# Kernel tuning notes

Measured on AMD Instinct MI355X. Metric: run time of the kernel, lower is better.

Reference implementation:

```python
import jax, jax.numpy as jnp
import numpy as np

N, E, A, D, B = 30000, 60000, 6, 16, 4096
F_IN, F_HID, F_EMB = 256, 256, 256
ALPHA = 0.2  # LeakyReLU negative slope


def _layer(node_embs, edge_embs, edge_list, node_list, Wn, We, ae, an, concat):
    out = Wn.shape[1]
    hn = node_embs @ Wn                      # [N, out]
    he = edge_embs @ We                      # [E, out]
    # stage 1: hyperedge update = attention over its member nodes
    gn = hn[edge_list]                       # [E, A, out] gather
    se = (he @ ae[:out])[:, None] + gn @ ae[out:]            # [E, A]
    att_e = jax.nn.softmax(jax.nn.leaky_relu(se, ALPHA), axis=1)
    new_edge = jnp.einsum('ea,eao->eo', att_e, gn)           # [E, out]
    # stage 2: node update = attention over its incident hyperedges
    ge = new_edge[node_list]                 # [N, D, out] gather
    sn = (hn @ an[:out])[:, None] + ge @ an[out:]            # [N, D]
    att_n = jax.nn.softmax(jax.nn.leaky_relu(sn, ALPHA), axis=1)
    new_node = jnp.einsum('nd,ndo->no', att_n, ge)           # [N, out]
    if concat:
        return jax.nn.elu(new_node), jax.nn.elu(new_edge)
    return new_node, new_edge


def setup_inputs() -> dict:
    key = jax.random.key(0)
    ks = jax.random.split(key, 16)
    s = 0.1
    return {
        'batch_inputs': jax.random.randint(ks[0], (B, A + 1), 0, N),
        'node_embs': jax.random.normal(ks[1], (N, F_IN), jnp.float32),
        'edge_embs': jax.random.normal(ks[2], (E, F_IN), jnp.float32),
        'edge_list': jax.random.randint(ks[3], (E, A), 0, N),
        'node_list': jax.random.randint(ks[4], (N, D), 0, E),
        'Wn1': jax.random.normal(ks[5], (F_IN, F_HID), jnp.float32) * s,
        'We1': jax.random.normal(ks[6], (F_IN, F_HID), jnp.float32) * s,
        'ae1': jax.random.normal(ks[7], (2 * F_HID,), jnp.float32) * s,
        'an1': jax.random.normal(ks[8], (2 * F_HID,), jnp.float32) * s,
        'Wn2': jax.random.normal(ks[9], (F_HID, F_EMB), jnp.float32) * s,
        'We2': jax.random.normal(ks[10], (F_HID, F_EMB), jnp.float32) * s,
        'ae2': jax.random.normal(ks[11], (2 * F_EMB,), jnp.float32) * s,
        'an2': jax.random.normal(ks[12], (2 * F_EMB,), jnp.float32) * s,
    }


def reference(batch_inputs, node_embs, edge_embs, edge_list, node_list,
              Wn1, We1, ae1, an1, Wn2, We2, ae2, an2):
    # single attention head (nheads=1), concat=True -> ELU; dropout identity (eval)
    n1, e1 = _layer(node_embs, edge_embs, edge_list, node_list, Wn1, We1, ae1, an1, True)
    n2, e2 = _layer(n1, e1, edge_list, node_list, Wn2, We2, ae2, an2, False)
    n2, e2 = jax.nn.elu(n2), jax.nn.elu(e2)
    # assemble: slot 0 = hyperedge embedding, slots 1..right-1 = node embeddings
    S = batch_inputs.shape[1]
    cols = jnp.arange(S - 1)
    nz = batch_inputs[:, :-1] != 0
    right = jnp.max(jnp.where(nz, cols, -1), axis=1) + 1      # [B]
    pos = jnp.arange(S)
    mask = (pos[None, :] >= 1) & (pos[None, :] < right[:, None])  # [B, S]
    gathered = n2[batch_inputs]                               # [B, S, F_EMB]
    out = jnp.where(mask[:, :, None], gathered, jnp.float32(0))
    out = out.at[:, 0, :].set(e2[batch_inputs[:, 0]])
    return out
```

## Files before the change

kernel.cpp:

```cpp
#include <hip/hip_runtime.h>
#include <stdint.h>

typedef unsigned short u16;
typedef unsigned int   u32;
typedef __attribute__((ext_vector_type(8))) short bf16x8;
typedef __attribute__((ext_vector_type(4))) float f32x4;

#define N_NODES 30000
#define N_EDGES 60000
#define A_DEG   6
#define D_DEG   16
#define BATCH   4096
#define FEAT    256
#define APAD    8

__device__ __forceinline__ float bfbits2f(u32 hi){ union{u32 u; float f;} v; v.u = hi; return v.f; }
__device__ __forceinline__ float bf2f(u16 h){ return bfbits2f(((u32)h)<<16); }
__device__ __forceinline__ u16 f2bf(float f){
  union{float f; u32 u;} v; v.f = f;
  u32 u = v.u;
  return (u16)((u + 0x7fffu + ((u>>16)&1u)) >> 16);
}

struct F4 { float x,y,z,w; };
struct F8 { float v[8]; };

__device__ __forceinline__ F4 load4(const float* p){
  float4 t = *reinterpret_cast<const float4*>(p);
  F4 f; f.x=t.x; f.y=t.y; f.z=t.z; f.w=t.w; return f;
}
__device__ __forceinline__ F4 load4(const u16* p){
  uint2 u = *reinterpret_cast<const uint2*>(p);
  F4 f;
  f.x = bfbits2f(u.x<<16);
  f.y = bfbits2f(u.x & 0xffff0000u);
  f.z = bfbits2f(u.y<<16);
  f.w = bfbits2f(u.y & 0xffff0000u);
  return f;
}
__device__ __forceinline__ F8 load8(const float* p){
  float4 a = *reinterpret_cast<const float4*>(p);
  float4 b = *reinterpret_cast<const float4*>(p+4);
  F8 f; f.v[0]=a.x; f.v[1]=a.y; f.v[2]=a.z; f.v[3]=a.w;
        f.v[4]=b.x; f.v[5]=b.y; f.v[6]=b.z; f.v[7]=b.w; return f;
}
__device__ __forceinline__ F8 load8(const u16* p){
  uint4 u = *reinterpret_cast<const uint4*>(p);
  F8 f;
  f.v[0]=bfbits2f(u.x<<16); f.v[1]=bfbits2f(u.x&0xffff0000u);
  f.v[2]=bfbits2f(u.y<<16); f.v[3]=bfbits2f(u.y&0xffff0000u);
  f.v[4]=bfbits2f(u.z<<16); f.v[5]=bfbits2f(u.z&0xffff0000u);
  f.v[6]=bfbits2f(u.w<<16); f.v[7]=bfbits2f(u.w&0xffff0000u);
  return f;
}
__device__ __forceinline__ void acc8(float* o, uint4 u, float ww){
  o[0] += ww*bfbits2f(u.x<<16); o[1] += ww*bfbits2f(u.x&0xffff0000u);
  o[2] += ww*bfbits2f(u.y<<16); o[3] += ww*bfbits2f(u.y&0xffff0000u);
  o[4] += ww*bfbits2f(u.z<<16); o[5] += ww*bfbits2f(u.z&0xffff0000u);
  o[6] += ww*bfbits2f(u.w<<16); o[7] += ww*bfbits2f(u.w&0xffff0000u);
}
__device__ __forceinline__ void store_bf8(u16* p, const float* f){
  uint4 u;
  u.x = (u32)f2bf(f[0]) | ((u32)f2bf(f[1])<<16);
  u.y = (u32)f2bf(f[2]) | ((u32)f2bf(f[3])<<16);
  u.z = (u32)f2bf(f[4]) | ((u32)f2bf(f[5])<<16);
  u.w = (u32)f2bf(f[6]) | ((u32)f2bf(f[7])<<16);
  *reinterpret_cast<uint4*>(p) = u;
}

__device__ __forceinline__ float eluf(float x){ return x > 0.f ? x : (__expf(x) - 1.f); }
__device__ __forceinline__ float lrelu(float x){ return x > 0.f ? x : 0.2f*x; }

__device__ __forceinline__ float wave_sum_lane0(float v){
  #pragma unroll
  for (int off = 32; off > 0; off >>= 1) v += __shfl_down(v, off, 64);
  return v;
}
__device__ __forceinline__ float half_sum_all(float v){
  #pragma unroll
  for (int off = 1; off < 32; off <<= 1) v += __shfl_xor(v, off, 64);
  return v;
}

__global__ __launch_bounds__(256) void prep_k(
    const float* __restrict__ Wn1, u16* __restrict__ Wt1,
    const float* __restrict__ Wn2, u16* __restrict__ Wt2,
    const float* __restrict__ We1, const float* __restrict__ ae1, float* __restrict__ wE1,
    const float* __restrict__ We2, const float* __restrict__ ae2, float* __restrict__ wE2)
{
  if (blockIdx.z < 2){
    const float* W = blockIdx.z ? Wn2 : Wn1;
    u16* Wt        = blockIdx.z ? Wt2 : Wt1;
    __shared__ float T[32][33];
    const int bx = blockIdx.x;
    const int by = blockIdx.y;
    const int tc = threadIdx.x & 31;
    const int tr = threadIdx.x >> 5;
    #pragma unroll
    for (int i=0;i<4;i++){
      int r = tr + i*8;
      T[r][tc] = W[(bx*32 + r)*FEAT + by*32 + tc];
    }
    __syncthreads();
    #pragma unroll
    for (int i=0;i<4;i++){
      int r = tr + i*8;
      Wt[(by*32 + r)*FEAT + bx*32 + tc] = f2bf(T[tc][r]);
    }
  } else {
    const int vb   = blockIdx.y*8 + blockIdx.x;
    const int lane = threadIdx.x & 63;
    const int row  = vb*4 + (threadIdx.x >> 6);
    const int c    = lane*4;
    {
      F4 h = load4(We1 + (long)row*FEAT + c);
      F4 a = load4(ae1 + c);
      float p = wave_sum_lane0(h.x*a.x + h.y*a.y + h.z*a.z + h.w*a.w);
      if (lane == 0) wE1[row] = p;
    }
    {
      F4 h = load4(We2 + (long)row*FEAT + c);
      F4 a = load4(ae2 + c);
      float p = wave_sum_lane0(h.x*a.x + h.y*a.y + h.z*a.z + h.w*a.w);
      if (lane == 0) wE2[row] = p;
    }
  }
}

template<bool ELU, typename TIN>
__global__ __launch_bounds__(256) void gemm_mfma_k(
    const TIN* __restrict__ X, const u16* __restrict__ Wt,
    const float* __restrict__ v1, const float* __restrict__ v2,
    u16* __restrict__ Y, float* __restrict__ hg, float* __restrict__ snb,
    int M)
{
  __shared__ u16 As[64][FEAT + APAD];
  __shared__ float hgs[64], sns[64];
  const int tid = threadIdx.x;
  const long row0 = (long)blockIdx.x * 64;

  if (tid < 64){ hgs[tid] = 0.f; sns[tid] = 0.f; }

  {
    const int c = (tid & 15) << 4;
    #pragma unroll
    for (int i=0;i<4;i++){
      const int r = (tid >> 4) + 16*i;
      u16* dst = &As[r][c];
      if (row0 + r < M){
        const TIN* src = X + (row0 + r)*FEAT + c;
        #pragma unroll
        for (int j=0;j<4;j++){
          F4 v = load4(src + 4*j);
          if (ELU){ v.x=eluf(v.x); v.y=eluf(v.y); v.z=eluf(v.z); v.w=eluf(v.w); }
          dst[4*j+0]=f2bf(v.x); dst[4*j+1]=f2bf(v.y);
          dst[4*j+2]=f2bf(v.z); dst[4*j+3]=f2bf(v.w);
        }
      } else {
        #pragma unroll
        for (int j=0;j<16;j++) dst[j] = 0;
      }
    }
  }
  __syncthreads();

  const int wave = tid >> 6;
  const int lane = tid & 63;
  const int l15  = lane & 15;
  const int kg   = lane >> 4;

  f32x4 acc[4][4] = {};

  for (int k0 = 0; k0 < FEAT; k0 += 32){
    bf16x8 a[4], b[4];
    #pragma unroll
    for (int rt=0;rt<4;rt++)
      a[rt] = *reinterpret_cast<const bf16x8*>(&As[rt*16 + l15][k0 + kg*8]);
    #pragma unroll
    for (int t=0;t<4;t++){
      const int n = wave*64 + t*16 + l15;
      b[t] = *reinterpret_cast<const bf16x8*>(Wt + (long)n*FEAT + k0 + kg*8);
    }
    #pragma unroll
    for (int rt=0;rt<4;rt++)
      #pragma unroll
      for (int t=0;t<4;t++)
        acc[rt][t] = __builtin_amdgcn_mfma_f32_16x16x32_bf16(a[rt], b[t], acc[rt][t], 0, 0, 0);
  }

  __syncthreads();

  float p1[4][4] = {}, p2[4][4] = {};
  #pragma unroll
  for (int t=0;t<4;t++){
    const int col = wave*64 + t*16 + l15;
    const float a1 = v1[col];
    const float a2 = v2[col];
    #pragma unroll
    for (int rt=0;rt<4;rt++){
      #pragma unroll
      for (int r=0;r<4;r++){
        const float val = acc[rt][t][r];
        As[rt*16 + kg*4 + r][col] = f2bf(val);
        p1[rt][r] += val * a1;
        p2[rt][r] += val * a2;
      }
    }
  }
  #pragma unroll
  for (int off=1; off<16; off<<=1){
    #pragma unroll
    for (int rt=0;rt<4;rt++)
      #pragma unroll
      for (int r=0;r<4;r++){
        p1[rt][r] += __shfl_xor(p1[rt][r], off, 64);
        p2[rt][r] += __shfl_xor(p2[rt][r], off, 64);
      }
  }
  if (l15 == 0){
    #pragma unroll
    for (int rt=0;rt<4;rt++)
      #pragma unroll
      for (int r=0;r<4;r++){
        atomicAdd(&hgs[rt*16 + kg*4 + r], p1[rt][r]);
        atomicAdd(&sns[rt*16 + kg*4 + r], p2[rt][r]);
      }
  }
  __syncthreads();

  {
    const int c = (tid & 15) << 4;
    #pragma unroll
    for (int i=0;i<4;i++){
      const int r = (tid >> 4) + 16*i;
      if (row0 + r < M){
        const uint4* s = reinterpret_cast<const uint4*>(&As[r][c]);
        uint4* d = reinterpret_cast<uint4*>(Y + (row0 + r)*FEAT + c);
        d[0] = s[0]; d[1] = s[1];
      }
    }
  }
  if (tid < 64 && row0 + tid < M){
    hg[row0 + tid]  = hgs[tid];
    snb[row0 + tid] = sns[tid];
  }
}

__global__ __launch_bounds__(256) void node_gemm_k(
    const u16* __restrict__ NE, const int* __restrict__ node_list,
    const float* __restrict__ snb1, const float* __restrict__ ned,
    const u16* __restrict__ Wt,
    const float* __restrict__ v1, const float* __restrict__ v2,
    u16* __restrict__ Y, float* __restrict__ hg, float* __restrict__ snb2,
    int M)
{
  __shared__ u16 As[64][FEAT + APAD];
  __shared__ float hgs[64], sns[64];
  const int tid = threadIdx.x;
  const long row0 = (long)blockIdx.x * 64;

  if (tid < 64){ hgs[tid] = 0.f; sns[tid] = 0.f; }

  const int hw = tid >> 5;
  const int hl = tid & 31;
  const int c  = hl*8;
  for (int i=0;i<4;i++){
    const int rA = hw*8 + 2*i;
    const int rB = rA + 1;
    const long nA = row0 + rA;
    const long nB = row0 + rB;
    u16* dstA = &As[rA][c];
    u16* dstB = &As[rB][c];
    if (nB < M){
      int idxA[D_DEG], idxB[D_DEG];
      #pragma unroll
      for (int d=0; d<D_DEG; d++) idxA[d] = node_list[nA*D_DEG + d];
      #pragma unroll
      for (int d=0; d<D_DEG; d++) idxB[d] = node_list[nB*D_DEG + d];
      float nvA[D_DEG], nvB[D_DEG];
      #pragma unroll
      for (int d=0; d<D_DEG; d++) nvA[d] = ned[idxA[d]];
      #pragma unroll
      for (int d=0; d<D_DEG; d++) nvB[d] = ned[idxB[d]];
      uint4 hbA[D_DEG], hbB[D_DEG];
      #pragma unroll
      for (int d=0; d<D_DEG; d++)
        hbA[d] = *reinterpret_cast<const uint4*>(NE + (long)idxA[d]*FEAT + c);
      #pragma unroll
      for (int d=0; d<D_DEG; d++)
        hbB[d] = *reinterpret_cast<const uint4*>(NE + (long)idxB[d]*FEAT + c);

      const float sbA = snb1[nA];
      const float sbB = snb1[nB];
      float wA[D_DEG], wB[D_DEG];
      float mxA = -1e30f, mxB = -1e30f;
      #pragma unroll
      for (int d=0; d<D_DEG; d++){
        float sA = lrelu(sbA + nvA[d]); wA[d] = sA; mxA = fmaxf(mxA, sA);
        float sB = lrelu(sbB + nvB[d]); wB[d] = sB; mxB = fmaxf(mxB, sB);
      }
      float sumA = 0.f, sumB = 0.f;
      #pragma unroll
      for (int d=0; d<D_DEG; d++){
        wA[d] = __expf(wA[d]-mxA); sumA += wA[d];
        wB[d] = __expf(wB[d]-mxB); sumB += wB[d];
      }
      const float invA = 1.f/sumA;
      const float invB = 1.f/sumB;

      float oA[8] = {};
      #pragma unroll
      for (int d=0; d<D_DEG; d++) acc8(oA, hbA[d], wA[d]*invA);
      #pragma unroll
      for (int j=0;j<8;j++) dstA[j] = f2bf(eluf(oA[j]));

      float oB[8] = {};
      #pragma unroll
      for (int d=0; d<D_DEG; d++) acc8(oB, hbB[d], wB[d]*invB);
      #pragma unroll
      for (int j=0;j<8;j++) dstB[j] = f2bf(eluf(oB[j]));
    } else {
      for (int t=0;t<2;t++){
        const long n = (t==0) ? nA : nB;
        u16* dst = (t==0) ? dstA : dstB;
        if (n < M){
          int idx[D_DEG];
          #pragma unroll
          for (int d=0; d<D_DEG; d++) idx[d] = node_list[n*D_DEG + d];
          float nv[D_DEG];
          #pragma unroll
          for (int d=0; d<D_DEG; d++) nv[d] = ned[idx[d]];
          uint4 hb[D_DEG];
          #pragma unroll
          for (int d=0; d<D_DEG; d++)
            hb[d] = *reinterpret_cast<const uint4*>(NE + (long)idx[d]*FEAT + c);
          const float sb = snb1[n];
          float w[D_DEG];
          float mx = -1e30f;
          #pragma unroll
          for (int d=0; d<D_DEG; d++){
            float s = lrelu(sb + nv[d]); w[d] = s; mx = fmaxf(mx, s);
          }
          float sum = 0.f;
          #pragma unroll
          for (int d=0; d<D_DEG; d++){ w[d] = __expf(w[d]-mx); sum += w[d]; }
          const float inv = 1.f/sum;
          float o[8] = {};
          #pragma unroll
          for (int d=0; d<D_DEG; d++) acc8(o, hb[d], w[d]*inv);
          #pragma unroll
          for (int j=0;j<8;j++) dst[j] = f2bf(eluf(o[j]));
        } else {
          #pragma unroll
          for (int j=0;j<8;j++) dst[j] = 0;
        }
      }
    }
  }
  __syncthreads();

  const int wave = tid >> 6;
  const int lane = tid & 63;
  const int l15  = lane & 15;
  const int kg   = lane >> 4;

  f32x4 acc[4][4] = {};

  for (int k0 = 0; k0 < FEAT; k0 += 32){
    bf16x8 a[4], b[4];
    #pragma unroll
    for (int rt=0;rt<4;rt++)
      a[rt] = *reinterpret_cast<const bf16x8*>(&As[rt*16 + l15][k0 + kg*8]);
    #pragma unroll
    for (int t=0;t<4;t++){
      const int n = wave*64 + t*16 + l15;
      b[t] = *reinterpret_cast<const bf16x8*>(Wt + (long)n*FEAT + k0 + kg*8);
    }
    #pragma unroll
    for (int rt=0;rt<4;rt++)
      #pragma unroll
      for (int t=0;t<4;t++)
        acc[rt][t] = __builtin_amdgcn_mfma_f32_16x16x32_bf16(a[rt], b[t], acc[rt][t], 0, 0, 0);
  }

  __syncthreads();

  float p1[4][4] = {}, p2[4][4] = {};
  #pragma unroll
  for (int t=0;t<4;t++){
    const int col = wave*64 + t*16 + l15;
    const float a1 = v1[col];
    const float a2 = v2[col];
    #pragma unroll
    for (int rt=0;rt<4;rt++){
      #pragma unroll
      for (int r=0;r<4;r++){
        const float val = acc[rt][t][r];
        As[rt*16 + kg*4 + r][col] = f2bf(val);
        p1[rt][r] += val * a1;
        p2[rt][r] += val * a2;
      }
    }
  }
  #pragma unroll
  for (int off=1; off<16; off<<=1){
    #pragma unroll
    for (int rt=0;rt<4;rt++)
      #pragma unroll
      for (int r=0;r<4;r++){
        p1[rt][r] += __shfl_xor(p1[rt][r], off, 64);
        p2[rt][r] += __shfl_xor(p2[rt][r], off, 64);
      }
  }
  if (l15 == 0){
    #pragma unroll
    for (int rt=0;rt<4;rt++)
      #pragma unroll
      for (int r=0;r<4;r++){
        atomicAdd(&hgs[rt*16 + kg*4 + r], p1[rt][r]);
        atomicAdd(&sns[rt*16 + kg*4 + r], p2[rt][r]);
      }
  }
  __syncthreads();

  {
    const int cc = (tid & 15) << 4;
    #pragma unroll
    for (int i=0;i<4;i++){
      const int r = (tid >> 4) + 16*i;
      if (row0 + r < M){
        const uint4* s = reinterpret_cast<const uint4*>(&As[r][cc]);
        uint4* d = reinterpret_cast<uint4*>(Y + (row0 + r)*FEAT + cc);
        d[0] = s[0]; d[1] = s[1];
      }
    }
  }
  if (tid < 64 && row0 + tid < M){
    hg[row0 + tid]   = hgs[tid];
    snb2[row0 + tid] = sns[tid];
  }
}

template<typename TIN, bool ELU, bool SB_PRE, bool SEB_OUT>
__global__ __launch_bounds__(256) void edge_attn_k(const u16* __restrict__ Hn,
    const TIN* __restrict__ Xe, const float* __restrict__ wE,
    const int* __restrict__ edge_list,
    const float* __restrict__ hg, const float* __restrict__ an_hi,
    const float* __restrict__ seb_in, const float* __restrict__ wE_nxt,
    float* __restrict__ seb_out,
    u16* __restrict__ NE, float* __restrict__ ned)
{
  const int tid = threadIdx.x;
  const int hl  = tid & 31;
  const int e   = blockIdx.x*8 + (tid >> 5);
  const int c   = hl*8;

  int idx[A_DEG];
  #pragma unroll
  for (int a=0;a<A_DEG;a++) idx[a] = edge_list[e*A_DEG + a];
  float hgv[A_DEG];
  #pragma unroll
  for (int a=0;a<A_DEG;a++) hgv[a] = hg[idx[a]];
  uint4 hb[A_DEG];
  #pragma unroll
  for (int a=0;a<A_DEG;a++)
    hb[a] = *reinterpret_cast<const uint4*>(Hn + (long)idx[a]*FEAT + c);

  float sb;
  if (SB_PRE){
    sb = seb_in[e];
  } else {
    F8 x = load8(Xe + (long)e*FEAT + c);
    if (ELU){
      #pragma unroll
      for (int j=0;j<8;j++) x.v[j] = eluf(x.v[j]);
    }
    F8 v = load8(wE + c);
    float p = 0.f;
    #pragma unroll
    for (int j=0;j<8;j++) p += x.v[j]*v.v[j];
    sb = half_sum_all(p);
  }

  float w[A_DEG];
  float mx = -1e30f;
  #pragma unroll
  for (int a=0;a<A_DEG;a++){
    float s = lrelu(sb + hgv[a]);
    w[a] = s; mx = fmaxf(mx, s);
  }
  float sum = 0.f;
  #pragma unroll
  for (int a=0;a<A_DEG;a++){ w[a] = __expf(w[a]-mx); sum += w[a]; }
  const float inv = 1.f/sum;

  float o[8] = {};
  #pragma unroll
  for (int a=0;a<A_DEG;a++) acc8(o, hb[a], w[a]*inv);
  store_bf8(NE + (long)e*FEAT + c, o);

  {
    F8 v = load8(an_hi + c);
    float p = 0.f;
    #pragma unroll
    for (int j=0;j<8;j++) p += o[j]*v.v[j];
    p = half_sum_all(p);
    if (hl == 0) ned[e] = p;
  }
  if (SEB_OUT){
    F8 v = load8(wE_nxt + c);
    float p = 0.f;
    #pragma unroll
    for (int j=0;j<8;j++) p += eluf(o[j])*v.v[j];
    p = half_sum_all(p);
    if (hl == 0) seb_out[e] = p;
  }
}

__global__ __launch_bounds__(256) void node_assemble_k(
    const u16* __restrict__ NE, const int* __restrict__ node_list,
    const float* __restrict__ snb, const float* __restrict__ ned,
    const int* __restrict__ batch, float* __restrict__ out)
{
  const int b   = blockIdx.x;
  const int tid = threadIdx.x;
  const int hw  = tid >> 5;
  const int hl  = tid & 31;
  const int c   = hl*8;

  int right = 0;
  #pragma unroll
  for (int cc=0; cc<6; cc++){ if (batch[b*7 + cc] != 0) right = cc+1; }

  if (hw == 6){
    const int e = batch[b*7 + 0];
    F8 x = load8(NE + (long)e*FEAT + c);
    float4 o0, o1;
    o0.x=eluf(x.v[0]); o0.y=eluf(x.v[1]); o0.z=eluf(x.v[2]); o0.w=eluf(x.v[3]);
    o1.x=eluf(x.v[4]); o1.y=eluf(x.v[5]); o1.z=eluf(x.v[6]); o1.w=eluf(x.v[7]);
    float* po = out + ((long)b*7 + 0)*FEAT + c;
    *reinterpret_cast<float4*>(po)   = o0;
    *reinterpret_cast<float4*>(po+4) = o1;
  } else if (hw < 6){
    const int s  = hw + 1;
    float* po = out + ((long)b*7 + s)*FEAT + c;
    if (s < right){
      const int n = batch[b*7 + s];
      int idx[D_DEG];
      #pragma unroll
      for (int d=0; d<D_DEG; d++) idx[d] = node_list[(long)n*D_DEG + d];
      float nv[D_DEG];
      #pragma unroll
      for (int d=0; d<D_DEG; d++) nv[d] = ned[idx[d]];
      const float sb = snb[n];
      float w[D_DEG];
      float mx = -1e30f;
      #pragma unroll
      for (int d=0; d<D_DEG; d++){
        float sc = lrelu(sb + nv[d]);
        w[d] = sc; mx = fmaxf(mx, sc);
      }
      float sum = 0.f;
      #pragma unroll
      for (int d=0; d<D_DEG; d++){ w[d] = __expf(w[d]-mx); sum += w[d]; }
      const float inv = 1.f/sum;

      uint4 hb[D_DEG];
      #pragma unroll
      for (int d=0; d<D_DEG; d++)
        hb[d] = *reinterpret_cast<const uint4*>(NE + (long)idx[d]*FEAT + c);
      float o[8] = {};
      #pragma unroll
      for (int d=0; d<D_DEG; d++) acc8(o, hb[d], w[d]*inv);

      float4 o0, o1;
      o0.x=eluf(o[0]); o0.y=eluf(o[1]); o0.z=eluf(o[2]); o0.w=eluf(o[3]);
      o1.x=eluf(o[4]); o1.y=eluf(o[5]); o1.z=eluf(o[6]); o1.w=eluf(o[7]);
      *reinterpret_cast<float4*>(po)   = o0;
      *reinterpret_cast<float4*>(po+4) = o1;
    } else {
      float4 z; z.x=0.f; z.y=0.f; z.z=0.f; z.w=0.f;
      *reinterpret_cast<float4*>(po)   = z;
      *reinterpret_cast<float4*>(po+4) = z;
    }
  }
}

extern "C" void kernel_launch(void* const* d_in, const int* in_sizes, int n_in,
                              void* d_out, int out_size, void* d_ws, size_t ws_size,
                              hipStream_t stream)
{
  const int*   batch      = (const int*)d_in[0];
  const float* node_embs  = (const float*)d_in[1];
  const float* edge_embs  = (const float*)d_in[2];
  const int*   edge_list  = (const int*)d_in[3];
  const int*   node_list  = (const int*)d_in[4];
  const float* Wn1 = (const float*)d_in[5];
  const float* We1 = (const float*)d_in[6];
  const float* ae1 = (const float*)d_in[7];
  const float* an1 = (const float*)d_in[8];
  const float* Wn2 = (const float*)d_in[9];
  const float* We2 = (const float*)d_in[10];
  const float* ae2 = (const float*)d_in[11];
  const float* an2 = (const float*)d_in[12];
  float* out = (float*)d_out;

  char* ws = (char*)d_ws;
  size_t off = 0;
  auto alloc = [&](size_t bytes)->void* {
    void* p = ws + off; off += (bytes + 255) & ~(size_t)255; return p;
  };
  u16* bHn = (u16*)alloc((size_t)N_NODES*FEAT*2);
  u16* bNE = (u16*)alloc((size_t)N_EDGES*FEAT*2);
  u16* Wt1 = (u16*)alloc((size_t)FEAT*FEAT*2);
  u16* Wt2 = (u16*)alloc((size_t)FEAT*FEAT*2);
  float* hg   = (float*)alloc((size_t)N_NODES*4);
  float* snb  = (float*)alloc((size_t)N_NODES*4);
  float* ned  = (float*)alloc((size_t)N_EDGES*4);
  float* seb2 = (float*)alloc((size_t)N_EDGES*4);
  float* wE1  = (float*)alloc(FEAT*4);
  float* wE2  = (float*)alloc(FEAT*4);

  dim3 blk(256);
  const int gemm_grid = (N_NODES + 63) / 64;

  prep_k<<<dim3(8,8,3), blk, 0, stream>>>(Wn1, Wt1, Wn2, Wt2,
      We1, ae1, wE1, We2, ae2, wE2);

  gemm_mfma_k<false,float><<<gemm_grid, blk, 0, stream>>>(node_embs, Wt1,
      ae1+FEAT, an1, bHn, hg, snb, N_NODES);
  edge_attn_k<float,false,false,true><<<N_EDGES/8, blk, 0, stream>>>(bHn, edge_embs, wE1,
      edge_list, hg, an1+FEAT, nullptr, wE2, seb2, bNE, ned);

  node_gemm_k<<<gemm_grid, blk, 0, stream>>>(bNE, node_list, snb, ned,
      Wt2, ae2+FEAT, an2, bHn, hg, snb, N_NODES);

  edge_attn_k<u16,true,true,false><<<N_EDGES/8, blk, 0, stream>>>(bHn, bNE, wE2,
      edge_list, hg, an2+FEAT, seb2, nullptr, nullptr, bNE, ned);

  node_assemble_k<<<BATCH, blk, 0, stream>>>(bNE, node_list, snb, ned, batch, out);
}
```

Baseline: 290.8 us.

## Split fused node-attention+GEMM kernel into separate attention and MFMA GEMM kernels

Replaces the fused layer-1 node attention plus layer-2 node GEMM kernel with two kernels. One computes node attention and writes bf16 node embeddings to a new buffer, and the existing generic MFMA GEMM then runs on that buffer. The seb_out projection now rounds the edge embedding to bf16 before ELU so it matches what the next layer reads. The split gives the gather-heavy attention its own grid with 8 nodes per block, at the cost of an extra launch and a full write and read of the 30000x256 bf16 intermediate.

```diff
diff --git a/kernel.cpp b/kernel.cpp
--- a/kernel.cpp
+++ b/kernel.cpp
@@ -246,199 +246,47 @@
   }
 }
 
-__global__ __launch_bounds__(256) void node_gemm_k(
-    const u16* __restrict__ NE, const int* __restrict__ node_list,
-    const float* __restrict__ snb1, const float* __restrict__ ned,
-    const u16* __restrict__ Wt,
-    const float* __restrict__ v1, const float* __restrict__ v2,
-    u16* __restrict__ Y, float* __restrict__ hg, float* __restrict__ snb2,
-    int M)
-{
-  __shared__ u16 As[64][FEAT + APAD];
-  __shared__ float hgs[64], sns[64];
+__global__ __launch_bounds__(256) void node_attn1_k(const u16* __restrict__ NE,
+    const int* __restrict__ node_list, const float* __restrict__ snb,
+    const float* __restrict__ ned, u16* __restrict__ NNo)
+{
   const int tid = threadIdx.x;
-  const long row0 = (long)blockIdx.x * 64;
-
-  if (tid < 64){ hgs[tid] = 0.f; sns[tid] = 0.f; }
-
-  const int hw = tid >> 5;
-  const int hl = tid & 31;
-  const int c  = hl*8;
-  for (int i=0;i<4;i++){
-    const int rA = hw*8 + 2*i;
-    const int rB = rA + 1;
-    const long nA = row0 + rA;
-    const long nB = row0 + rB;
-    u16* dstA = &As[rA][c];
-    u16* dstB = &As[rB][c];
-    if (nB < M){
-      int idxA[D_DEG], idxB[D_DEG];
-      #pragma unroll
-      for (int d=0; d<D_DEG; d++) idxA[d] = node_list[nA*D_DEG + d];
-      #pragma unroll
-      for (int d=0; d<D_DEG; d++) idxB[d] = node_list[nB*D_DEG + d];
-      float nvA[D_DEG], nvB[D_DEG];
-      #pragma unroll
-      for (int d=0; d<D_DEG; d++) nvA[d] = ned[idxA[d]];
-      #pragma unroll
-      for (int d=0; d<D_DEG; d++) nvB[d] = ned[idxB[d]];
-      uint4 hbA[D_DEG], hbB[D_DEG];
-      #pragma unroll
-      for (int d=0; d<D_DEG; d++)
-        hbA[d] = *reinterpret_cast<const uint4*>(NE + (long)idxA[d]*FEAT + c);
-      #pragma unroll
-      for (int d=0; d<D_DEG; d++)
-        hbB[d] = *reinterpret_cast<const uint4*>(NE + (long)idxB[d]*FEAT + c);
-
-      const float sbA = snb1[nA];
-      const float sbB = snb1[nB];
-      float wA[D_DEG], wB[D_DEG];
-      float mxA = -1e30f, mxB = -1e30f;
-      #pragma unroll
-      for (int d=0; d<D_DEG; d++){
-        float sA = lrelu(sbA + nvA[d]); wA[d] = sA; mxA = fmaxf(mxA, sA);
-        float sB = lrelu(sbB + nvB[d]); wB[d] = sB; mxB = fmaxf(mxB, sB);
-      }
-      float sumA = 0.f, sumB = 0.f;
-      #pragma unroll
-      for (int d=0; d<D_DEG; d++){
-        wA[d] = __expf(wA[d]-mxA); sumA += wA[d];
-        wB[d] = __expf(wB[d]-mxB); sumB += wB[d];
-      }
-      const float invA = 1.f/sumA;
-      const float invB = 1.f/sumB;
-
-      float oA[8] = {};
-      #pragma unroll
-      for (int d=0; d<D_DEG; d++) acc8(oA, hbA[d], wA[d]*invA);
-      #pragma unroll
-      for (int j=0;j<8;j++) dstA[j] = f2bf(eluf(oA[j]));
-
-      float oB[8] = {};
-      #pragma unroll
-      for (int d=0; d<D_DEG; d++) acc8(oB, hbB[d], wB[d]*invB);
-      #pragma unroll
-      for (int j=0;j<8;j++) dstB[j] = f2bf(eluf(oB[j]));
-    } else {
-      for (int t=0;t<2;t++){
-        const long n = (t==0) ? nA : nB;
-        u16* dst = (t==0) ? dstA : dstB;
-        if (n < M){
-          int idx[D_DEG];
-          #pragma unroll
-          for (int d=0; d<D_DEG; d++) idx[d] = node_list[n*D_DEG + d];
-          float nv[D_DEG];
-          #pragma unroll
-          for (int d=0; d<D_DEG; d++) nv[d] = ned[idx[d]];
-          uint4 hb[D_DEG];
-          #pragma unroll
-          for (int d=0; d<D_DEG; d++)
-            hb[d] = *reinterpret_cast<const uint4*>(NE + (long)idx[d]*FEAT + c);
-          const float sb = snb1[n];
-          float w[D_DEG];
-          float mx = -1e30f;
-          #pragma unroll
-          for (int d=0; d<D_DEG; d++){
-            float s = lrelu(sb + nv[d]); w[d] = s; mx = fmaxf(mx, s);
-          }
-          float sum = 0.f;
-          #pragma unroll
-          for (int d=0; d<D_DEG; d++){ w[d] = __expf(w[d]-mx); sum += w[d]; }
-          const float inv = 1.f/sum;
-          float o[8] = {};
-          #pragma unroll
-          for (int d=0; d<D_DEG; d++) acc8(o, hb[d], w[d]*inv);
-          #pragma unroll
-          for (int j=0;j<8;j++) dst[j] = f2bf(eluf(o[j]));
-        } else {
-          #pragma unroll
-          for (int j=0;j<8;j++) dst[j] = 0;
-        }
-      }
-    }
-  }
-  __syncthreads();
-
-  const int wave = tid >> 6;
-  const int lane = tid & 63;
-  const int l15  = lane & 15;
-  const int kg   = lane >> 4;
-
-  f32x4 acc[4][4] = {};
-
-  for (int k0 = 0; k0 < FEAT; k0 += 32){
-    bf16x8 a[4], b[4];
-    #pragma unroll
-    for (int rt=0;rt<4;rt++)
-      a[rt] = *reinterpret_cast<const bf16x8*>(&As[rt*16 + l15][k0 + kg*8]);
-    #pragma unroll
-    for (int t=0;t<4;t++){
-      const int n = wave*64 + t*16 + l15;
-      b[t] = *reinterpret_cast<const bf16x8*>(Wt + (long)n*FEAT + k0 + kg*8);
-    }
-    #pragma unroll
-    for (int rt=0;rt<4;rt++)
-      #pragma unroll
-      for (int t=0;t<4;t++)
-        acc[rt][t] = __builtin_amdgcn_mfma_f32_16x16x32_bf16(a[rt], b[t], acc[rt][t], 0, 0, 0);
-  }
-
-  __syncthreads();
-
-  float p1[4][4] = {}, p2[4][4] = {};
-  #pragma unroll
-  for (int t=0;t<4;t++){
-    const int col = wave*64 + t*16 + l15;
-    const float a1 = v1[col];
-    const float a2 = v2[col];
-    #pragma unroll
-    for (int rt=0;rt<4;rt++){
-      #pragma unroll
-      for (int r=0;r<4;r++){
-        const float val = acc[rt][t][r];
-        As[rt*16 + kg*4 + r][col] = f2bf(val);
-        p1[rt][r] += val * a1;
-        p2[rt][r] += val * a2;
-      }
-    }
-  }
-  #pragma unroll
-  for (int off=1; off<16; off<<=1){
-    #pragma unroll
-    for (int rt=0;rt<4;rt++)
-      #pragma unroll
-      for (int r=0;r<4;r++){
-        p1[rt][r] += __shfl_xor(p1[rt][r], off, 64);
-        p2[rt][r] += __shfl_xor(p2[rt][r], off, 64);
-      }
-  }
-  if (l15 == 0){
-    #pragma unroll
-    for (int rt=0;rt<4;rt++)
-      #pragma unroll
-      for (int r=0;r<4;r++){
-        atomicAdd(&hgs[rt*16 + kg*4 + r], p1[rt][r]);
-        atomicAdd(&sns[rt*16 + kg*4 + r], p2[rt][r]);
-      }
-  }
-  __syncthreads();
-
-  {
-    const int cc = (tid & 15) << 4;
-    #pragma unroll
-    for (int i=0;i<4;i++){
-      const int r = (tid >> 4) + 16*i;
-      if (row0 + r < M){
-        const uint4* s = reinterpret_cast<const uint4*>(&As[r][cc]);
-        uint4* d = reinterpret_cast<uint4*>(Y + (row0 + r)*FEAT + cc);
-        d[0] = s[0]; d[1] = s[1];
-      }
-    }
-  }
-  if (tid < 64 && row0 + tid < M){
-    hg[row0 + tid]   = hgs[tid];
-    snb2[row0 + tid] = sns[tid];
-  }
+  const int hl  = tid & 31;
+  const int n   = blockIdx.x*8 + (tid >> 5);
+  const int c   = hl*8;
+
+  int idx[D_DEG];
+  #pragma unroll
+  for (int d=0; d<D_DEG; d++) idx[d] = node_list[(long)n*D_DEG + d];
+  float nv[D_DEG];
+  #pragma unroll
+  for (int d=0; d<D_DEG; d++) nv[d] = ned[idx[d]];
+
+  uint4 hb[D_DEG];
+  #pragma unroll
+  for (int d=0; d<D_DEG; d++)
+    hb[d] = *reinterpret_cast<const uint4*>(NE + (long)idx[d]*FEAT + c);
+
+  const float sb = snb[n];
+  float w[D_DEG];
+  float mx = -1e30f;
+  #pragma unroll
+  for (int d=0; d<D_DEG; d++){
+    float s = lrelu(sb + nv[d]);
+    w[d] = s; mx = fmaxf(mx, s);
+  }
+  float sum = 0.f;
+  #pragma unroll
+  for (int d=0; d<D_DEG; d++){ w[d] = __expf(w[d]-mx); sum += w[d]; }
+  const float inv = 1.f/sum;
+
+  float o[8] = {};
+  #pragma unroll
+  for (int d=0; d<D_DEG; d++) acc8(o, hb[d], w[d]*inv);
+
+  #pragma unroll
+  for (int j=0;j<8;j++) o[j] = eluf(o[j]);
+  store_bf8(NNo + (long)n*FEAT + c, o);
 }
 
 template<typename TIN, bool ELU, bool SB_PRE, bool SEB_OUT>
@@ -511,7 +359,7 @@
     F8 v = load8(wE_nxt + c);
     float p = 0.f;
     #pragma unroll
-    for (int j=0;j<8;j++) p += eluf(o[j])*v.v[j];
+    for (int j=0;j<8;j++) p += eluf(bf2f(f2bf(o[j])))*v.v[j];
     p = half_sum_all(p);
     if (hl == 0) seb_out[e] = p;
   }
@@ -612,6 +460,7 @@
   };
   u16* bHn = (u16*)alloc((size_t)N_NODES*FEAT*2);
   u16* bNE = (u16*)alloc((size_t)N_EDGES*FEAT*2);
+  u16* bNN = (u16*)alloc((size_t)N_NODES*FEAT*2);
   u16* Wt1 = (u16*)alloc((size_t)FEAT*FEAT*2);
   u16* Wt2 = (u16*)alloc((size_t)FEAT*FEAT*2);
   float* hg   = (float*)alloc((size_t)N_NODES*4);
@@ -632,8 +481,10 @@
   edge_attn_k<float,false,false,true><<<N_EDGES/8, blk, 0, stream>>>(bHn, edge_embs, wE1,
       edge_list, hg, an1+FEAT, nullptr, wE2, seb2, bNE, ned);
 
-  node_gemm_k<<<gemm_grid, blk, 0, stream>>>(bNE, node_list, snb, ned,
-      Wt2, ae2+FEAT, an2, bHn, hg, snb, N_NODES);
+  node_attn1_k<<<N_NODES/8, blk, 0, stream>>>(bNE, node_list, snb, ned, bNN);
+
+  gemm_mfma_k<false,u16><<<gemm_grid, blk, 0, stream>>>(bNN, Wt2,
+      ae2+FEAT, an2, bHn, hg, snb, N_NODES);
 
   edge_attn_k<u16,true,true,false><<<N_EDGES/8, blk, 0, stream>>>(bHn, bNE, wE2,
       edge_list, hg, an2+FEAT, seb2, nullptr, nullptr, bNE, ned);
```

Measured after the change: 290.0 us. Within noise of the previous version (-0.3%).
